# Kernel optimization log

Hardware: AMD Instinct MI355X
Metric: run time of the kernel (lower is better)

## Reference

```python
import jax, jax.numpy as jnp
import numpy as np

N = 131072        # total nodes
D = 256           # d_model (params.emb_dim)
STEPS = 16        # depth steps
G = N // STEPS    # nodes per depth step (equal-sized groups)
B = 16            # batch (number of trees); all lengths equal N//B
V = 1024          # len(id2word)
# op schedule: -1 leaf embedding, -2 numeric encoder, 0/1 unary ('sin','cos'), 2/3 binary ('add','mul')
SCHEDULE = [-1, -2, 0, 2, 1, 3, 0, 2, 1, 3, 0, 2, 1, 3, 0, 2]


def setup_inputs() -> dict:
    key = jax.random.key(0)
    ks = jax.random.split(key, 8)
    tokens = jax.random.randint(ks[0], (N,), 0, V, dtype=jnp.int32)
    # children of a node at depth d must already be computed: indices < d*G
    rng = np.random.default_rng(0)
    li = np.zeros(N, np.int32)
    ri = np.zeros(N, np.int32)
    for d in range(2, STEPS):
        li[d * G:(d + 1) * G] = rng.integers(0, d * G, G)
        ri[d * G:(d + 1) * G] = rng.integers(0, d * G, G)
    depths = jnp.repeat(jnp.arange(STEPS, dtype=jnp.int32), G)
    operation_order = jnp.array(SCHEDULE, dtype=jnp.int32)
    lengths = jnp.full((B,), N // B, dtype=jnp.int32)
    s = 0.05
    leaf_table = jax.random.normal(ks[1], (V, D), jnp.float32)
    num_W1 = jax.random.normal(ks[2], (D, 1), jnp.float32) * s
    num_b1 = jnp.zeros((D,), jnp.float32)
    num_W2 = jax.random.normal(ks[3], (D, D), jnp.float32) * s
    num_b2 = jnp.zeros((D,), jnp.float32)
    una_W = jax.random.normal(ks[4], (2, 4, D, D), jnp.float32) * s
    una_b = jnp.zeros((2, 4, D), jnp.float32)
    bin_W = jax.random.normal(ks[5], (2, 10, D, D), jnp.float32) * s
    bin_b = jnp.zeros((2, 5, D), jnp.float32)
    return dict(tokens=tokens, left_idx=jnp.asarray(li), right_idx=jnp.asarray(ri),
                depths=depths, operation_order=operation_order, lengths=lengths,
                leaf_table=leaf_table, num_W1=num_W1, num_b1=num_b1,
                num_W2=num_W2, num_b2=num_b2,
                una_W=una_W, una_b=una_b, bin_W=bin_W, bin_b=bin_b)


def _unary_cell(hc, W, b):
    # hc: [G, 2, D]; W: [4, D, D] (data, forget, output, input); b: [4, D]
    h, c = hc[:, 0], hc[:, 1]
    g = jnp.einsum('nd,ked->kne', h, W) + b[:, None, :]  # y = h @ W_k.T + b_k
    i = jax.nn.sigmoid(g[0])
    f = jax.nn.sigmoid(g[1])
    o = jax.nn.sigmoid(g[2])
    u = jnp.tanh(g[3])
    c2 = i * u + f * c
    h2 = o * jnp.tanh(c2)
    h2 = h2 / jnp.linalg.norm(h2)  # global (Frobenius) norm, as in torch h.norm(p=2)
    c2 = c2 / jnp.linalg.norm(c2)
    return jnp.stack([h2, c2], axis=1)


def _binary_cell(hcl, hcr, W, b):
    # W: [10, D, D] = (data_l, data_r, f_ll, f_lr, f_rl, f_rr, out_l, out_r, in_l, in_r)
    # b: [5, D] = (data, forget_l, forget_r, output, input)
    hl, cl = hcl[:, 0], hcl[:, 1]
    hr, cr = hcr[:, 0], hcr[:, 1]
    gl = jnp.einsum('nd,ked->kne', hl, W[jnp.array([0, 2, 4, 6, 8])])
    gr = jnp.einsum('nd,ked->kne', hr, W[jnp.array([1, 3, 5, 7, 9])])
    g = gl + gr + b[:, None, :]
    i = jax.nn.sigmoid(g[0])
    f_l = jax.nn.sigmoid(g[1])
    f_r = jax.nn.sigmoid(g[2])
    o = jax.nn.sigmoid(g[3])
    u = jnp.tanh(g[4])
    c2 = i * u + f_l * cl + f_r * cr
    h2 = o * jnp.tanh(c2)
    h2 = h2 / jnp.linalg.norm(h2)
    c2 = c2 / jnp.linalg.norm(c2)
    return jnp.stack([h2, c2], axis=1)


def reference(tokens, left_idx, right_idx, depths, operation_order, lengths,
              leaf_table, num_W1, num_b1, num_W2, num_b2,
              una_W, una_b, bin_W, bin_b):
    sched = np.asarray(operation_order).tolist()  # static dispatch schedule
    n = tokens.shape[0]
    steps = len(sched)
    g = n // steps
    d_model = leaf_table.shape[1]
    acts = jnp.zeros((n, 2, d_model), leaf_table.dtype)
    for d, op in enumerate(sched):
        s = d * g
        if op == -1:  # leaf embedding with max_norm=1.0 renorm (non-differentiable scale)
            e = leaf_table[tokens[s:s + g]]
            nrm = jnp.linalg.norm(e, axis=-1, keepdims=True)
            scale = jax.lax.stop_gradient(jnp.minimum(1.0, 1.0 / (nrm + 1e-7)))
            e = e * scale
            step_act = jnp.stack([e, jnp.zeros_like(e)], axis=1)
        elif op == -2:  # numeric encoder
            x = tokens[s:s + g].astype(leaf_table.dtype)[:, None]
            h1 = jax.nn.sigmoid(x @ num_W1.T + num_b1)
            e = jax.nn.sigmoid(h1 @ num_W2.T + num_b2)
            step_act = jnp.stack([e, jnp.zeros_like(e)], axis=1)
        elif op in (0, 1):  # unary LSTM cell: gather child then cell
            child = acts[left_idx[s:s + g]]
            step_act = _unary_cell(child, una_W[op], una_b[op])
        else:  # binary LSTM cell: gather both children
            l = acts[left_idx[s:s + g]]
            r = acts[right_idx[s:s + g]]
            step_act = _binary_cell(l, r, bin_W[op - 2], bin_b[op - 2])
        acts = jax.lax.dynamic_update_slice(acts, step_act, (s, 0, 0))
    hidden = acts[:, 0, :]  # [N, D]
    batch = lengths.shape[0]
    # all lengths equal -> pad_sequence is a reshape: [B, L, D]
    return hidden.reshape(batch, n // batch, d_model)
```

## Files before the change

kernel.cpp:

```cpp
#include <hip/hip_runtime.h>
#include <hip/hip_bf16.h>
#include <cstdint>

typedef unsigned short u16;
typedef unsigned int u32;
typedef __attribute__((ext_vector_type(4))) float floatx4;
typedef __attribute__((ext_vector_type(8))) short shortx8;

#define G_STEP 8192
#define N_TOTAL 131072
#define RHALF (1280*256)

__device__ __forceinline__ float bfu2f(u16 x){ return __uint_as_float(((unsigned)x)<<16); }
__device__ __forceinline__ u16 f2bfu(float x){ __hip_bfloat16 b = __float2bfloat16(x); return *reinterpret_cast<u16*>(&b); }
__device__ __forceinline__ float sigm(float x){ return 1.0f/(1.0f+__expf(-x)); }
__device__ __forceinline__ float tanh_(float x){
  float cx = fminf(fmaxf(x,-15.f),15.f);
  float e = __expf(2.f*cx);
  return (e-1.f)/(e+1.f);
}
__device__ __forceinline__ float invs(float x){ return 1.0f/sqrtf(x); }

__device__ __forceinline__ void gl16(const void* g, void* l){
  __builtin_amdgcn_global_load_lds((const __attribute__((address_space(1))) u32*)g,
                                   (__attribute__((address_space(3))) u32*)l, 16, 0, 0);
}

__device__ __forceinline__ void cvt8(const float* __restrict__ src, u16* __restrict__ dst){
  float4 a = *reinterpret_cast<const float4*>(src);
  float4 b = *reinterpret_cast<const float4*>(src+4);
  ushort4 o0; o0.x=f2bfu(a.x); o0.y=f2bfu(a.y); o0.z=f2bfu(a.z); o0.w=f2bfu(a.w);
  ushort4 o1; o1.x=f2bfu(b.x); o1.y=f2bfu(b.y); o1.z=f2bfu(b.z); o1.w=f2bfu(b.w);
  *reinterpret_cast<ushort4*>(dst)   = o0;
  *reinterpret_cast<ushort4*>(dst+4) = o1;
}

__global__ __launch_bounds__(256) void setup_kernel(
    const int* __restrict__ tokens, const float* __restrict__ leaf_table,
    const float* __restrict__ W1, const float* __restrict__ b1,
    const float* __restrict__ una_W, const float* __restrict__ bin_W,
    const float* __restrict__ num_W2,
    u16* __restrict__ wbu, u16* __restrict__ wbb, u16* __restrict__ wbn,
    u16* __restrict__ h1, u16* __restrict__ H, u16* __restrict__ C,
    float* __restrict__ sumsq)
{
  const int b = blockIdx.x, tid = threadIdx.x;
  if (b < 256){
    int row = b*8 + (tid>>5), d0 = (tid&31)*8;
    int op = row>>10, w = row&1023;
    int gate = (w>>4)&3, e = ((w>>6)<<4) | (w&15);
    cvt8(una_W + (size_t)((op*4+gate)*256 + e)*256 + d0, wbu + (size_t)row*256 + d0);
  } else if (b < 896){
    int row = (b-256)*8 + (tid>>5), d0 = (tid&31)*8;
    int ob = row / 2560, rem = row - ob*2560;
    int lr = rem / 1280, rw = rem - lr*1280;
    int eblk = rw / 80, rem2 = rw - eblk*80;
    int gate = rem2 >> 4, el = rem2 & 15;
    int e = eblk*16 + el;
    cvt8(bin_W + (size_t)((ob*10 + 2*gate + lr)*256 + e)*256 + d0, wbb + (size_t)row*256 + d0);
  } else if (b < 928){
    int row = (b-896)*8 + (tid>>5), d0 = (tid&31)*8;
    cvt8(num_W2 + (size_t)row*256 + d0, wbn + (size_t)row*256 + d0);
  } else if (b < 2976){
    int wave = tid >> 6, lane = tid & 63;
    int node = (b-928)*4 + wave;
    int t = tokens[node];
    const float4 e4 = *reinterpret_cast<const float4*>(leaf_table + (size_t)t*256 + lane*4);
    float ss = e4.x*e4.x + e4.y*e4.y + e4.z*e4.z + e4.w*e4.w;
    #pragma unroll
    for (int o = 32; o; o >>= 1) ss += __shfl_down(ss, o);
    ss = __shfl(ss, 0);
    float scale = fminf(1.0f, 1.0f/(sqrtf(ss) + 1e-7f));
    ushort4 hv;
    hv.x = f2bfu(e4.x*scale); hv.y = f2bfu(e4.y*scale);
    hv.z = f2bfu(e4.z*scale); hv.w = f2bfu(e4.w*scale);
    ushort4 zv; zv.x = zv.y = zv.z = zv.w = 0;
    *reinterpret_cast<ushort4*>(H + (size_t)node*256 + lane*4) = hv;
    *reinterpret_cast<ushort4*>(C + (size_t)node*256 + lane*4) = zv;
  } else if (b < 4000){
    int flat = (b-2976)*2048 + tid*8;
    int n = flat >> 8, d0 = flat & 255;
    float x = (float)tokens[G_STEP + n];
    float4 w0 = *reinterpret_cast<const float4*>(W1 + d0);
    float4 w1 = *reinterpret_cast<const float4*>(W1 + d0 + 4);
    float4 c0 = *reinterpret_cast<const float4*>(b1 + d0);
    float4 c1 = *reinterpret_cast<const float4*>(b1 + d0 + 4);
    ushort4 o0, o1;
    o0.x = f2bfu(sigm(x*w0.x + c0.x)); o0.y = f2bfu(sigm(x*w0.y + c0.y));
    o0.z = f2bfu(sigm(x*w0.z + c0.z)); o0.w = f2bfu(sigm(x*w0.w + c0.w));
    o1.x = f2bfu(sigm(x*w1.x + c1.x)); o1.y = f2bfu(sigm(x*w1.y + c1.y));
    o1.z = f2bfu(sigm(x*w1.z + c1.z)); o1.w = f2bfu(sigm(x*w1.w + c1.w));
    *reinterpret_cast<ushort4*>(h1 + flat)     = o0;
    *reinterpret_cast<ushort4*>(h1 + flat + 4) = o1;
  } else {
    if (tid < 32) sumsq[tid] = ((tid & 15) < 2) ? 1.0f : 0.0f;
  }
}

template<int MODE>
__global__ __launch_bounds__(256, 2) void gemm_fused(
    const u16* __restrict__ Asrc, const int* __restrict__ lidx,
    const int* __restrict__ ridx, const u16* __restrict__ Wb,
    const float* __restrict__ bias, const u16* __restrict__ Cin,
    float* __restrict__ sumsq, u16* __restrict__ H, u16* __restrict__ C,
    int sbase, int step)
{
  constexpr int NG  = (MODE==0) ? 1 : (MODE==1 ? 4 : 5);
  constexpr int NBR = (MODE==2) ? 160 : 128;
  constexpr int NT  = (MODE==2) ? 8 : 4;
  constexpr int BR  = NBR/32;
  constexpr int WN  = (MODE==2) ? 80 : 64;
  constexpr int NFR = WN/16;

  __shared__ u16 SA[2][128][64];
  __shared__ u16 SB[2][NBR][64];
  __shared__ float scH[16];
  __shared__ float scC[16];
  __shared__ float red[8];

  const int tid  = threadIdx.x;
  const int lane = tid & 63, wave = tid >> 6;
  const int mbase = blockIdx.x*128;
  const int nbase = blockIdx.y*NBR;
  const int l15 = lane & 15, kg = lane >> 4;
  const int rhi = lane >> 3;
  const int lc  = (lane & 7) ^ rhi;

  if (MODE != 0){
    if (tid < 16)           scH[tid]    = invs(sumsq[tid]);
    else if (tid < 32)      scC[tid-16] = invs(sumsq[tid]);
  }

  const u16* aL[4]; const u16* aR[4]; const u16* bP[BR];
  #pragma unroll
  for (int rr = 0; rr < 4; rr++){
    int r = rr*32 + wave*8 + rhi;
    int gr;
    if constexpr (MODE==0) gr = mbase + r;
    else                   gr = lidx[sbase + mbase + r];
    aL[rr] = Asrc + (size_t)gr*256 + lc*8;
    if constexpr (MODE==2)
      aR[rr] = Asrc + (size_t)ridx[sbase + mbase + r]*256 + lc*8;
  }
  #pragma unroll
  for (int rb = 0; rb < BR; rb++){
    int r = rb*32 + wave*8 + rhi;
    bP[rb] = Wb + (size_t)(nbase + r)*256 + lc*8;
  }

  floatx4 accL[4][NFR];
  #pragma unroll
  for (int i = 0; i < 4; i++)
    #pragma unroll
    for (int j = 0; j < NFR; j++) accL[i][j] = (floatx4)(0.0f);
  floatx4 accR[(MODE==2)?4:1][(MODE==2)?NFR:1];
  if constexpr (MODE==2){
    #pragma unroll
    for (int i = 0; i < 4; i++)
      #pragma unroll
      for (int j = 0; j < NFR; j++) accR[i][j] = (floatx4)(0.0f);
  }

  const int wm = (wave >> 1)*64, wn = (wave & 1)*WN;

  auto stage = [&](int t, int buf){
    const int kk = t*64;
    #pragma unroll
    for (int rr = 0; rr < 4; rr++){
      const u16* ga;
      if constexpr (MODE==2){ ga = (kk >= 256) ? aR[rr] + (kk-256) : aL[rr] + kk; }
      else                  { ga = aL[rr] + kk; }
      gl16(ga, &SA[buf][rr*32 + wave*8][0]);
    }
    #pragma unroll
    for (int rb = 0; rb < BR; rb++){
      const u16* gb;
      if constexpr (MODE==2){ gb = (kk >= 256) ? bP[rb] + RHALF + (kk-256) : bP[rb] + kk; }
      else                  { gb = bP[rb] + kk; }
      gl16(gb, &SB[buf][rb*32 + wave*8][0]);
    }
  };

  stage(0, 0);
  __syncthreads();

  #pragma unroll
  for (int t = 0; t < NT; t++){
    if (t+1 < NT) stage(t+1, (t+1)&1);
    const int buf = t & 1;
    #pragma unroll
    for (int j = 0; j < 2; j++){
      shortx8 af[4], bfr[NFR];
      const int pc = ((j*4 + kg) ^ (l15 & 7)) * 8;
      #pragma unroll
      for (int i = 0; i < 4; i++)
        af[i] = *reinterpret_cast<const shortx8*>(&SA[buf][wm + i*16 + l15][pc]);
      #pragma unroll
      for (int n = 0; n < NFR; n++)
        bfr[n] = *reinterpret_cast<const shortx8*>(&SB[buf][wn + n*16 + l15][pc]);
      if (MODE==2 && t >= 4){
        #pragma unroll
        for (int mi = 0; mi < 4; mi++)
          #pragma unroll
          for (int ni = 0; ni < NFR; ni++)
            accR[mi][ni] = __builtin_amdgcn_mfma_f32_16x16x32_bf16(af[mi], bfr[ni], accR[mi][ni], 0, 0, 0);
      } else {
        #pragma unroll
        for (int mi = 0; mi < 4; mi++)
          #pragma unroll
          for (int ni = 0; ni < NFR; ni++)
            accL[mi][ni] = __builtin_amdgcn_mfma_f32_16x16x32_bf16(af[mi], bfr[ni], accL[mi][ni], 0, 0, 0);
      }
    }
    __syncthreads();
  }

  if constexpr (MODE == 0){
    float bb[4];
    #pragma unroll
    for (int ni = 0; ni < 4; ni++) bb[ni] = bias[nbase + wn + ni*16 + l15];
    #pragma unroll
    for (int mi = 0; mi < 4; mi++){
      #pragma unroll
      for (int r = 0; r < 4; r++){
        int node = sbase + mbase + wm + mi*16 + kg*4 + r;
        u16* hp = H + (size_t)node*256 + nbase + wn + l15;
        u16* cp = C + (size_t)node*256 + nbase + wn + l15;
        #pragma unroll
        for (int ni = 0; ni < 4; ni++){
          hp[ni*16] = f2bfu(sigm(accL[mi][ni][r] + bb[ni]));
          cp[ni*16] = 0;
        }
      }
    }
  } else {
    const int eb = blockIdx.y*2 + (wave & 1);
    const int e  = eb*16 + l15;
    float bb[NG];
    #pragma unroll
    for (int g = 0; g < NG; g++) bb[g] = bias[g*256 + e];
    float hss = 0.f, css = 0.f;
    #pragma unroll
    for (int mi = 0; mi < 4; mi++){
      #pragma unroll
      for (int r = 0; r < 4; r++){
        int orow = mbase + wm + mi*16 + kg*4 + r;
        int node = sbase + orow;
        int chl = lidx[node];
        float sl = scH[chl >> 13];
        float cl = bfu2f(Cin[(size_t)chl*256 + e]) * scC[chl >> 13];
        float c2, h2;
        if constexpr (MODE == 1){
          float i_ = sigm(accL[mi][0][r]*sl + bb[0]);
          float f_ = sigm(accL[mi][1][r]*sl + bb[1]);
          float o_ = sigm(accL[mi][2][r]*sl + bb[2]);
          float u_ = tanh_(accL[mi][3][r]*sl + bb[3]);
          c2 = i_*u_ + f_*cl;
          h2 = o_*tanh_(c2);
        } else {
          int chr = ridx[node];
          float sr = scH[chr >> 13];
          float cr = bfu2f(Cin[(size_t)chr*256 + e]) * scC[chr >> 13];
          float g0 = accL[mi][0][r]*sl + accR[mi][0][r]*sr + bb[0];
          float g1 = accL[mi][1][r]*sl + accR[mi][1][r]*sr + bb[1];
          float g2 = accL[mi][2][r]*sl + accR[mi][2][r]*sr + bb[2];
          float g3 = accL[mi][3][r]*sl + accR[mi][3][r]*sr + bb[3];
          float g4 = accL[mi][4][r]*sl + accR[mi][4][r]*sr + bb[4];
          float i_ = sigm(g0);
          float fl = sigm(g1);
          float fr = sigm(g2);
          float o_ = sigm(g3);
          float u_ = tanh_(g4);
          c2 = i_*u_ + fl*cl + fr*cr;
          h2 = o_*tanh_(c2);
        }
        H[(size_t)node*256 + e] = f2bfu(h2);
        C[(size_t)node*256 + e] = f2bfu(c2);
        hss += h2*h2;
        css += c2*c2;
      }
    }
    #pragma unroll
    for (int o = 32; o; o >>= 1){ hss += __shfl_down(hss, o); css += __shfl_down(css, o); }
    if (lane == 0){ red[wave] = hss; red[4+wave] = css; }
    __syncthreads();
    if (tid == 0)  atomicAdd(&sumsq[step],      red[0]+red[1]+red[2]+red[3]);
    if (tid == 64) atomicAdd(&sumsq[16 + step], red[4]+red[5]+red[6]+red[7]);
  }
}

__global__ __launch_bounds__(256) void out_kernel(
    const u16* __restrict__ H, const float* __restrict__ sumsq, float* __restrict__ out)
{
  size_t base = ((size_t)blockIdx.x*256 + threadIdx.x)*8;
  int n = (int)(base >> 8);
  float s = invs(sumsq[n >> 13]);
  const uint4 v = *reinterpret_cast<const uint4*>(H + base);
  float4 o0, o1;
  o0.x = bfu2f((u16)(v.x & 0xffff))*s; o0.y = bfu2f((u16)(v.x >> 16))*s;
  o0.z = bfu2f((u16)(v.y & 0xffff))*s; o0.w = bfu2f((u16)(v.y >> 16))*s;
  o1.x = bfu2f((u16)(v.z & 0xffff))*s; o1.y = bfu2f((u16)(v.z >> 16))*s;
  o1.z = bfu2f((u16)(v.w & 0xffff))*s; o1.w = bfu2f((u16)(v.w >> 16))*s;
  *reinterpret_cast<float4*>(out + base)     = o0;
  *reinterpret_cast<float4*>(out + base + 4) = o1;
}

extern "C" void kernel_launch(void* const* d_in, const int* in_sizes, int n_in,
                              void* d_out, int out_size, void* d_ws, size_t ws_size,
                              hipStream_t stream)
{
  const int*   tokens     = (const int*)d_in[0];
  const int*   lidx       = (const int*)d_in[1];
  const int*   ridx       = (const int*)d_in[2];
  const float* leaf_table = (const float*)d_in[6];
  const float* num_W1     = (const float*)d_in[7];
  const float* num_b1     = (const float*)d_in[8];
  const float* num_W2     = (const float*)d_in[9];
  const float* num_b2     = (const float*)d_in[10];
  const float* una_W      = (const float*)d_in[11];
  const float* una_b      = (const float*)d_in[12];
  const float* bin_W      = (const float*)d_in[13];
  const float* bin_b      = (const float*)d_in[14];

  char* ws = (char*)d_ws;
  size_t off = 0;
  u16* H   = (u16*)(ws + off); off += (size_t)N_TOTAL*256*2;
  u16* wbu = (u16*)(ws + off); off += (size_t)2048*256*2;
  u16* wbb = (u16*)(ws + off); off += (size_t)5120*256*2;
  u16* wbn = (u16*)(ws + off); off += (size_t)256*256*2;
  u16* h1  = (u16*)(ws + off); off += (size_t)G_STEP*256*2;
  float* sumsq = (float*)(ws + off); off += 32*4;

  u16* C = (u16*)d_out;

  setup_kernel<<<4001, 256, 0, stream>>>(tokens, leaf_table, num_W1, num_b1,
                                         una_W, bin_W, num_W2,
                                         wbu, wbb, wbn, h1, H, C, sumsq);
  gemm_fused<0><<<dim3(64, 2), 256, 0, stream>>>(
      h1, nullptr, nullptr, wbn, num_b2, nullptr, sumsq, H, C, G_STEP, 1);

  const int sched[16] = {-1,-2,0,2,1,3,0,2,1,3,0,2,1,3,0,2};
  for (int d = 2; d < 16; d++){
    int op = sched[d];
    int sbase = d*G_STEP;
    if (op == 0 || op == 1){
      gemm_fused<1><<<dim3(64, 8), 256, 0, stream>>>(
          H, lidx, nullptr, wbu + (size_t)op*1024*256,
          una_b + (size_t)op*4*256, C, sumsq, H, C, sbase, d);
    } else {
      int o2 = op - 2;
      gemm_fused<2><<<dim3(64, 8), 256, 0, stream>>>(
          H, lidx, ridx, wbb + (size_t)o2*2*1280*256,
          bin_b + (size_t)o2*5*256, C, sumsq, H, C, sbase, d);
    }
  }
  out_kernel<<<(N_TOTAL*256)/(256*8), 256, 0, stream>>>(H, sumsq, (float*)d_out);
}
```

Before: 381.7 us.

## Prefetch two K-tiles ahead with explicit vmcnt waits and split barriers

```diff
diff --git a/kernel.cpp b/kernel.cpp
--- a/kernel.cpp
+++ b/kernel.cpp
@@ -25,6 +25,12 @@
   __builtin_amdgcn_global_load_lds((const __attribute__((address_space(1))) u32*)g,
                                    (__attribute__((address_space(3))) u32*)l, 16, 0, 0);
 }
+
+template<int V> __device__ __forceinline__ void wait_vm();
+template<> __device__ __forceinline__ void wait_vm<0>(){ asm volatile("s_waitcnt vmcnt(0)" ::: "memory"); }
+template<> __device__ __forceinline__ void wait_vm<8>(){ asm volatile("s_waitcnt vmcnt(8)" ::: "memory"); }
+template<> __device__ __forceinline__ void wait_vm<9>(){ asm volatile("s_waitcnt vmcnt(9)" ::: "memory"); }
+__device__ __forceinline__ void wait_lgkm0(){ asm volatile("s_waitcnt lgkmcnt(0)" ::: "memory"); }
 
 __device__ __forceinline__ void cvt8(const float* __restrict__ src, u16* __restrict__ dst){
   float4 a = *reinterpret_cast<const float4*>(src);
@@ -111,6 +117,7 @@
   constexpr int BR  = NBR/32;
   constexpr int WN  = (MODE==2) ? 80 : 64;
   constexpr int NFR = WN/16;
+  constexpr int LPS = 4 + BR;
 
   __shared__ u16 SA[2][128][64];
   __shared__ u16 SB[2][NBR][64];
@@ -182,16 +189,17 @@
   };
 
   stage(0, 0);
-  __syncthreads();
+  stage(1, 1);
+  if constexpr (LPS == 8) asm volatile("s_waitcnt vmcnt(8) lgkmcnt(0)" ::: "memory");
+  else                    asm volatile("s_waitcnt vmcnt(9) lgkmcnt(0)" ::: "memory");
+  __builtin_amdgcn_s_barrier();
 
   #pragma unroll
   for (int t = 0; t < NT; t++){
-    if (t+1 < NT) stage(t+1, (t+1)&1);
     const int buf = t & 1;
-    #pragma unroll
-    for (int j = 0; j < 2; j++){
+    {
       shortx8 af[4], bfr[NFR];
-      const int pc = ((j*4 + kg) ^ (l15 & 7)) * 8;
+      const int pc = (kg ^ (l15 & 7)) * 8;
       #pragma unroll
       for (int i = 0; i < 4; i++)
         af[i] = *reinterpret_cast<const shortx8*>(&SA[buf][wm + i*16 + l15][pc]);
@@ -212,7 +220,36 @@
             accL[mi][ni] = __builtin_amdgcn_mfma_f32_16x16x32_bf16(af[mi], bfr[ni], accL[mi][ni], 0, 0, 0);
       }
     }
-    __syncthreads();
+    {
+      shortx8 af[4], bfr[NFR];
+      const int pc = ((4 + kg) ^ (l15 & 7)) * 8;
+      #pragma unroll
+      for (int i = 0; i < 4; i++)
+        af[i] = *reinterpret_cast<const shortx8*>(&SA[buf][wm + i*16 + l15][pc]);
+      #pragma unroll
+      for (int n = 0; n < NFR; n++)
+        bfr[n] = *reinterpret_cast<const shortx8*>(&SB[buf][wn + n*16 + l15][pc]);
+      wait_lgkm0();
+      __builtin_amdgcn_s_barrier();
+      if (t + 2 < NT) stage(t+2, buf);
+      if (MODE==2 && t >= 4){
+        #pragma unroll
+        for (int mi = 0; mi < 4; mi++)
+          #pragma unroll
+          for (int ni = 0; ni < NFR; ni++)
+            accR[mi][ni] = __builtin_amdgcn_mfma_f32_16x16x32_bf16(af[mi], bfr[ni], accR[mi][ni], 0, 0, 0);
+      } else {
+        #pragma unroll
+        for (int mi = 0; mi < 4; mi++)
+          #pragma unroll
+          for (int ni = 0; ni < NFR; ni++)
+            accL[mi][ni] = __builtin_amdgcn_mfma_f32_16x16x32_bf16(af[mi], bfr[ni], accL[mi][ni], 0, 0, 0);
+      }
+    }
+    if (t + 1 < NT){
+      if (t + 2 < NT) wait_vm<LPS>(); else wait_vm<0>();
+      __builtin_amdgcn_s_barrier();
+    }
   }
 
   if constexpr (MODE == 0){
```

New measurement: 369.5 us. 3.2% less time.
